# Performance work log

Measured on AMD Instinct MI355X. Metric: run time of the kernel, lower is better.

Reference implementation:

```python
import jax, jax.numpy as jnp
import numpy as np

WS = 16         # window size
NH = 16         # num heads
EPS = 1e-6


def _ln(x):
    m = jnp.mean(x, axis=-1, keepdims=True)
    v = jnp.var(x, axis=-1, keepdims=True)
    return (x - m) * jax.lax.rsqrt(v + EPS)


def _modulate(x, shift, scale):
    return x * (1.0 + scale[:, None, :]) + shift[:, None, :]


def setup_inputs() -> dict:
    key = jax.random.key(0)
    ks = jax.random.split(key, 14)
    D, HD = 1024, 64
    s = 0.02
    return {
        'x': jax.random.normal(ks[0], (4, 4096, D), jnp.float32),
        'c': jax.random.normal(ks[1], (4, D), jnp.float32),
        'qkv_w': jax.random.normal(ks[2], (3 * D, D), jnp.float32) * s,
        'qkv_b': jax.random.normal(ks[3], (3 * D,), jnp.float32) * s,
        'proj_w': jax.random.normal(ks[4], (D, D), jnp.float32) * s,
        'proj_b': jax.random.normal(ks[5], (D,), jnp.float32) * s,
        'rel_pos_h': jax.random.normal(ks[6], (2 * WS - 1, HD), jnp.float32) * s,
        'rel_pos_w': jax.random.normal(ks[7], (2 * WS - 1, HD), jnp.float32) * s,
        'adaLN_w': jax.random.normal(ks[8], (6 * D, D), jnp.float32) * s,
        'adaLN_b': jax.random.normal(ks[9], (6 * D,), jnp.float32) * s,
        'fc1_w': jax.random.normal(ks[10], (4 * D, D), jnp.float32) * s,
        'fc1_b': jax.random.normal(ks[11], (4 * D,), jnp.float32) * s,
        'fc2_w': jax.random.normal(ks[12], (D, 4 * D), jnp.float32) * s,
        'fc2_b': jax.random.normal(ks[13], (D,), jnp.float32) * s,
    }


def _window_attention(x, qkv_w, qkv_b, proj_w, proj_b, rel_pos_h, rel_pos_w):
    # x: [N, T, D] with T = h*w, h = w = sqrt(T)
    N, T, D = x.shape
    h = w = int(round(T ** 0.5))
    nwh, nww = h // WS, w // WS  # grid divides evenly -> no padding
    hd = D // NH
    scale = hd ** -0.5

    # window partition: [N, h, w, D] -> [B, WS, WS, D], B = N*nwh*nww
    xw = x.reshape(N, nwh, WS, nww, WS, D).transpose(0, 1, 3, 2, 4, 5)
    xw = xw.reshape(N * nwh * nww, WS, WS, D)
    B = xw.shape[0]
    L = WS * WS

    qkv = (xw.reshape(B, L, D) @ qkv_w.T + qkv_b)  # [B, L, 3D]
    qkv = qkv.reshape(B, L, 3, NH, hd).transpose(2, 0, 3, 1, 4)  # [3, B, NH, L, hd]
    qkv = qkv.reshape(3, B * NH, L, hd)
    q, k, v = qkv[0], qkv[1], qkv[2]

    attn = jnp.einsum('bqc,bkc->bqk', q * scale, k)  # [B*NH, L, L]

    # decomposed relative position bias (q_size == k_size == WS)
    coords = jnp.arange(WS)
    rel_idx = coords[:, None] - coords[None, :] + (WS - 1)  # [WS, WS]
    Rh = rel_pos_h[rel_idx]  # [WS(q_h), WS(k_h), hd]
    Rw = rel_pos_w[rel_idx]  # [WS(q_w), WS(k_w), hd]
    rq = q.reshape(B * NH, WS, WS, hd)
    rel_h = jnp.einsum('bhwc,hkc->bhwk', rq, Rh)  # [B*NH, WS, WS, WS(kh)]
    rel_w = jnp.einsum('bhwc,wkc->bhwk', rq, Rw)  # [B*NH, WS, WS, WS(kw)]
    attn = (attn.reshape(B * NH, WS, WS, WS, WS)
            + rel_h[:, :, :, :, None]
            + rel_w[:, :, :, None, :]).reshape(B * NH, L, L)

    probs = jax.nn.softmax(attn, axis=-1)
    out = probs @ v  # [B*NH, L, hd]
    out = out.reshape(B, NH, WS, WS, hd).transpose(0, 2, 3, 1, 4).reshape(B, WS, WS, D)
    out = out @ proj_w.T + proj_b

    # window unpartition: [B, WS, WS, D] -> [N, T, D]
    out = out.reshape(N, nwh, nww, WS, WS, D).transpose(0, 1, 3, 2, 4, 5)
    return out.reshape(N, T, D)


def reference(x, c, qkv_w, qkv_b, proj_w, proj_b, rel_pos_h, rel_pos_w,
              adaLN_w, adaLN_b, fc1_w, fc1_b, fc2_w, fc2_b):
    D = x.shape[-1]
    mod = jax.nn.silu(c) @ adaLN_w.T + adaLN_b  # [N, 6D]
    sh_msa, sc_msa, g_msa, sh_mlp, sc_mlp, g_mlp = jnp.split(mod, 6, axis=1)

    a_in = _modulate(_ln(x), sh_msa, sc_msa)
    a_out = _window_attention(a_in, qkv_w, qkv_b, proj_w, proj_b, rel_pos_h, rel_pos_w)
    x = x + g_msa[:, None, :] * a_out

    m_in = _modulate(_ln(x), sh_mlp, sc_mlp)
    hdn = jax.nn.gelu(m_in @ fc1_w.T + fc1_b, approximate=True)
    m_out = hdn @ fc2_w.T + fc2_b
    x = x + g_mlp[:, None, :] * m_out
    return x
```

## Files before the change

### kernel.cpp

```cpp
#include <hip/hip_runtime.h>
#include <cstdint>
#include <cstddef>


typedef float  f32x4    __attribute__((ext_vector_type(4)));
typedef __bf16 bf16x8_t __attribute__((ext_vector_type(8)));
typedef __bf16 bf16x4_t __attribute__((ext_vector_type(4)));

#define DEV __device__ __forceinline__

DEV void gload_lds16(const void* g, void* l) {
    auto gp = (const uint32_t __attribute__((address_space(1)))*)(uintptr_t)g;
    auto lp = (uint32_t __attribute__((address_space(3)))*)(uint32_t)(uintptr_t)l;
    __builtin_amdgcn_global_load_lds(gp, lp, 16, 0, 0);
}

DEV bf16x8_t lds_frag(const __bf16* base, int row, int chunk, int row_elems) {
    return *(const bf16x8_t*)(base + row * row_elems + ((chunk ^ (row & 7)) << 3));
}

DEV bf16x8_t p_frag(const __bf16* base, int row, int chunk) {
    return *(const bf16x8_t*)(base + row * 32 + ((chunk ^ ((row >> 1) & 3)) << 3));
}

DEV int vt_addr(int d, int k) {
    return d * 64 + ((((k >> 3) ^ (d & 7) ^ ((d >> 3) & 7)) << 3) | (k & 7));
}

DEV float gelu_tanh(float v) {
    float u = 0.7978845608028654f * (v + 0.044715f * v * v * v);
    float e = __expf(2.f * u);
    float th = 1.f - 2.f / (e + 1.f);
    return 0.5f * v * (1.f + th);
}

DEV int win2tok(int r) {
    int nb = r >> 12, wi = (r >> 8) & 15, l = r & 255;
    return (nb << 12) + (wi >> 2) * 1024 + (l >> 4) * 64 + (wi & 3) * 16 + (l & 15);
}

__global__ void silu_k(const float* __restrict__ c, float* __restrict__ o, int n) {
    int i = blockIdx.x * 256 + threadIdx.x;
    if (i < n) { float v = c[i]; o[i] = v / (1.f + __expf(-v)); }
}

__global__ void zero_k(float* o, int n) {
    int i = blockIdx.x * 256 + threadIdx.x;
    if (i < n) o[i] = 0.f;
}

__global__ void conv_bf16(const float* __restrict__ s, __bf16* __restrict__ d, int n4) {
    int i = blockIdx.x * 256 + threadIdx.x;
    if (i < n4) {
        float4 v = ((const float4*)s)[i];
        bf16x4_t o; o[0] = (__bf16)v.x; o[1] = (__bf16)v.y; o[2] = (__bf16)v.z; o[3] = (__bf16)v.w;
        ((bf16x4_t*)d)[i] = o;
    }
}

__global__ __launch_bounds__(256)
void mod_gemv(const float* __restrict__ sc, const float* __restrict__ w,
              const float* __restrict__ b, float* __restrict__ mod) {
    int o = (blockIdx.x << 2) + (threadIdx.x >> 6);
    int lane = threadIdx.x & 63;
    int n = o / 6144, col = o % 6144;
    const float4* wr = (const float4*)(w + (size_t)col * 1024);
    const float4* sr = (const float4*)(sc + n * 1024);
    float acc = 0.f;
    #pragma unroll 4
    for (int i = lane; i < 256; i += 64) {
        float4 a = wr[i], x = sr[i];
        acc += a.x * x.x + a.y * x.y + a.z * x.z + a.w * x.w;
    }
    #pragma unroll
    for (int m = 1; m < 64; m <<= 1) acc += __shfl_xor(acc, m);
    if (lane == 0) mod[o] = acc + b[col];
}

__global__ __launch_bounds__(256)
void ln_mod_k(const float* __restrict__ src, const float* __restrict__ mod,
              int sh_off, int sc_off, __bf16* __restrict__ out, int permute, int r0) {
    int rl = blockIdx.x;
    int r = rl + r0;
    int nb = r >> 12;
    int t = permute ? win2tok(r) : r;
    float4 v = ((const float4*)(src + (size_t)t * 1024))[threadIdx.x];
    float s  = v.x + v.y + v.z + v.w;
    float sq = v.x * v.x + v.y * v.y + v.z * v.z + v.w * v.w;
    #pragma unroll
    for (int m = 1; m < 64; m <<= 1) { s += __shfl_xor(s, m); sq += __shfl_xor(sq, m); }
    __shared__ float ps[4], pq[4];
    int wv = threadIdx.x >> 6, ln = threadIdx.x & 63;
    if (ln == 0) { ps[wv] = s; pq[wv] = sq; }
    __syncthreads();
    s  = ps[0] + ps[1] + ps[2] + ps[3];
    sq = pq[0] + pq[1] + pq[2] + pq[3];
    float mean = s * (1.f / 1024.f);
    float var  = sq * (1.f / 1024.f) - mean * mean;
    float rstd = rsqrtf(var + 1e-6f);
    int c = threadIdx.x << 2;
    const float* mrow = mod + nb * 6144;
    float4 scv = *(const float4*)(mrow + sc_off + c);
    float4 shv = *(const float4*)(mrow + sh_off + c);
    bf16x4_t o;
    o[0] = (__bf16)((v.x - mean) * rstd * (1.f + scv.x) + shv.x);
    o[1] = (__bf16)((v.y - mean) * rstd * (1.f + scv.y) + shv.y);
    o[2] = (__bf16)((v.z - mean) * rstd * (1.f + scv.z) + shv.z);
    o[3] = (__bf16)((v.w - mean) * rstd * (1.f + scv.w) + shv.w);
    *(bf16x4_t*)(out + (size_t)rl * 1024 + c) = o;
}

template <int PM, int PN>
DEV void mfma16(f32x4 (&acc)[8][4], bf16x8_t (&fa)[4][2], bf16x8_t (&fb)[2][2][2]) {
    #pragma unroll
    for (int ks = 0; ks < 2; ++ks)
        #pragma unroll
        for (int mi = 0; mi < 4; ++mi)
            #pragma unroll
            for (int nn = 0; nn < 2; ++nn)
                acc[PM * 4 + mi][PN * 2 + nn] = __builtin_amdgcn_mfma_f32_16x16x32_bf16(
                    fa[mi][ks], fb[PN][nn][ks], acc[PM * 4 + mi][PN * 2 + nn], 0, 0, 0);
}

#define GBAR  __builtin_amdgcn_s_barrier()
#define LGKM0 do { asm volatile("s_waitcnt lgkmcnt(0)" ::: "memory"); \
                   __builtin_amdgcn_sched_barrier(0); } while (0)
#define PRIO1 __builtin_amdgcn_s_setprio(1)
#define PRIO0 __builtin_amdgcn_s_setprio(0)

template <int EPI>
__global__ __launch_bounds__(512)
void gemm256(const __bf16* __restrict__ A, const __bf16* __restrict__ B,
             const float* __restrict__ bias, void* __restrict__ Cout,
             const float* __restrict__ extra, const float* __restrict__ mod,
             int N, int K, int r0, int gx) {
    extern __shared__ __align__(16) char smem[];
    __bf16* lA = (__bf16*)smem;
    __bf16* lB = lA + 2 * 16384;
    const int tid = threadIdx.x, lane = tid & 63, wv = tid >> 6;
    const int wr = wv >> 2, wc = wv & 3;

    const int nwg = gridDim.x;
    const int qq = nwg >> 3, rr8 = nwg & 7;
    const int xcd = blockIdx.x & 7, pos = blockIdx.x >> 3;
    const int nid = (xcd < rr8 ? xcd * (qq + 1) : rr8 * (qq + 1) + (xcd - rr8) * qq) + pos;
    const int bm = (nid / gx) << 8, bn = (nid % gx) << 8;

    f32x4 acc[8][4];
    const f32x4 z4 = {0.f, 0.f, 0.f, 0.f};
    #pragma unroll
    for (int i = 0; i < 8; ++i)
        #pragma unroll
        for (int j = 0; j < 4; ++j) acc[i][j] = z4;

    bf16x8_t fa[4][2], fb[2][2][2];

    const int l8  = lane >> 3;
    const int gc8 = ((lane & 7) ^ l8) << 3;
    const int rbw = ((wv & 3) << 3) + ((wv >> 2) << 6);
    const __bf16* gA0 = A + (size_t)(bm +       (wv << 3) + l8) * K + gc8;
    const __bf16* gA1 = A + (size_t)(bm + 128 + (wv << 3) + l8) * K + gc8;
    const __bf16* gA2 = A + (size_t)(bm +  64 + (wv << 3) + l8) * K + gc8;
    const __bf16* gA3 = A + (size_t)(bm + 192 + (wv << 3) + l8) * K + gc8;
    const __bf16* gB0 = B + (size_t)(bn +       rbw + l8) * K + gc8;
    const __bf16* gB1 = B + (size_t)(bn + 128 + rbw + l8) * K + gc8;
    const __bf16* gB2 = B + (size_t)(bn +  32 + rbw + l8) * K + gc8;
    const __bf16* gB3 = B + (size_t)(bn + 160 + rbw + l8) * K + gc8;
    const int dA0 = (wv << 3) * 64, dA1 = (128 + (wv << 3)) * 64;
    const int dA2 = (64 + (wv << 3)) * 64, dA3 = (192 + (wv << 3)) * 64;
    const int dB0 = rbw * 64, dB1 = (128 + rbw) * 64;
    const int dB2 = (32 + rbw) * 64, dB3 = (160 + rbw) * 64;

    auto stA0 = [&](int be) { gload_lds16(gA0, lA + be + dA0); gload_lds16(gA1, lA + be + dA1); gA0 += 64; gA1 += 64; };
    auto stA1 = [&](int be) { gload_lds16(gA2, lA + be + dA2); gload_lds16(gA3, lA + be + dA3); gA2 += 64; gA3 += 64; };
    auto stB0 = [&](int be) { gload_lds16(gB0, lB + be + dB0); gload_lds16(gB1, lB + be + dB1); gB0 += 64; gB1 += 64; };
    auto stB1 = [&](int be) { gload_lds16(gB2, lB + be + dB2); gload_lds16(gB3, lB + be + dB3); gB2 += 64; gB3 += 64; };

    const int swzb = (lane >> 4) ^ (lane & 7);
    const __bf16* aR0 = lA + (wr << 13) + ((lane & 15) << 6) + (swzb << 3);
    const __bf16* aR1 = lA + (wr << 13) + ((lane & 15) << 6) + ((swzb ^ 4) << 3);
    const __bf16* bR0 = lB + (wc << 12) + ((lane & 15) << 6) + (swzb << 3);
    const __bf16* bR1 = lB + (wc << 12) + ((lane & 15) << 6) + ((swzb ^ 4) << 3);

    auto readA = [&](int be, int pm) {
        #pragma unroll
        for (int mi = 0; mi < 4; ++mi) {
            fa[mi][0] = *(const bf16x8_t*)(aR0 + be + pm * 4096 + mi * 1024);
            fa[mi][1] = *(const bf16x8_t*)(aR1 + be + pm * 4096 + mi * 1024);
        }
    };
    auto readB = [&](int be, int pn) {
        #pragma unroll
        for (int ni = 0; ni < 2; ++ni) {
            fb[pn][ni][0] = *(const bf16x8_t*)(bR0 + be + pn * 2048 + ni * 1024);
            fb[pn][ni][1] = *(const bf16x8_t*)(bR1 + be + pn * 2048 + ni * 1024);
        }
    };

    const int nt = K >> 6;
    stA0(0); stB0(0); stB1(0); stA1(0);
    stA0(16384); stB0(16384); stB1(16384);
    asm volatile("s_waitcnt vmcnt(6)" ::: "memory");
    GBAR;

    int be = 0;
    for (int t = 0; t < nt - 1; ++t) {
        const bool s2 = (t + 2 < nt);
        readA(be, 0); readB(be, 0);
        stA1(be ^ 16384);
        GBAR; LGKM0;
        PRIO1; mfma16<0, 0>(acc, fa, fb); PRIO0;
        GBAR;
        readB(be, 1);
        if (s2) stA0(be);
        GBAR; LGKM0;
        PRIO1; mfma16<0, 1>(acc, fa, fb); PRIO0;
        GBAR;
        readA(be, 1);
        if (s2) stB0(be);
        GBAR; LGKM0;
        PRIO1; mfma16<1, 0>(acc, fa, fb); PRIO0;
        GBAR;
        if (s2) stB1(be);
        if (t == nt - 2) asm volatile("s_waitcnt vmcnt(0)" ::: "memory");
        else             asm volatile("s_waitcnt vmcnt(6)" ::: "memory");
        GBAR;
        PRIO1; mfma16<1, 1>(acc, fa, fb); PRIO0;
        GBAR;
        be ^= 16384;
    }
    readA(be, 0); readB(be, 0); readB(be, 1);
    LGKM0;
    PRIO1; mfma16<0, 0>(acc, fa, fb); mfma16<0, 1>(acc, fa, fb); PRIO0;
    readA(be, 1);
    LGKM0;
    PRIO1; mfma16<1, 0>(acc, fa, fb); mfma16<1, 1>(acc, fa, fb); PRIO0;

    #pragma unroll
    for (int am = 0; am < 8; ++am) {
        #pragma unroll
        for (int j = 0; j < 4; ++j) {
            int m = bm + (wr << 7) + (am << 4) + ((lane >> 4) << 2) + j;
            #pragma unroll
            for (int an = 0; an < 4; ++an) {
                int n = bn + (wc << 6) + (an << 4) + (lane & 15);
                float v = acc[am][an][j] + bias[n];
                if constexpr (EPI == 0) {
                    ((__bf16*)Cout)[(size_t)m * N + n] = (__bf16)v;
                } else if constexpr (EPI == 1) {
                    int mg = m + r0;
                    int tr = win2tok(mg);
                    float g = mod[(mg >> 12) * 6144 + 2048 + n];
                    ((float*)Cout)[(size_t)tr * 1024 + n] = extra[(size_t)tr * 1024 + n] + g * v;
                } else if constexpr (EPI == 2) {
                    ((__bf16*)Cout)[(size_t)m * N + n] = (__bf16)gelu_tanh(v);
                } else {
                    int mg = m + r0;
                    float g = mod[(mg >> 12) * 6144 + 5120 + n];
                    ((float*)Cout)[(size_t)mg * 1024 + n] = extra[(size_t)mg * 1024 + n] + g * v;
                }
            }
        }
    }
}

__global__ __launch_bounds__(256)
void tab_k(const __bf16* __restrict__ qkv, const float* __restrict__ relh,
           const float* __restrict__ relw, __bf16* __restrict__ tab) {
    __shared__ __bf16 lR[2][31][72];
    for (int i = threadIdx.x; i < 1984; i += 256) {
        int row = i >> 6, c = i & 63;
        lR[0][row][c] = (__bf16)relh[i];
        lR[1][row][c] = (__bf16)relw[i];
    }
    __syncthreads();
    const int h = blockIdx.y;
    const int r = threadIdx.x >> 1, half = threadIdx.x & 1;
    const int l = blockIdx.x * 128 + r;
    const int lw = l & 255;
    const int qi = lw >> 4, qj = lw & 15;
    const __bf16* qrow = qkv + (size_t)l * 3072 + h * 64;
    float qq[64];
    #pragma unroll
    for (int c8 = 0; c8 < 8; ++c8) {
        bf16x8_t q8 = *(const bf16x8_t*)(qrow + (c8 << 3));
        #pragma unroll
        for (int e = 0; e < 8; ++e) qq[c8 * 8 + e] = (float)q8[e];
    }
    bf16x8_t oh, ow;
    #pragma unroll
    for (int kk = 0; kk < 8; ++kk) {
        int kg = (half << 3) + kk;
        const __bf16* Rh = &lR[0][qi - kg + 15][0];
        const __bf16* Rw = &lR[1][qj - kg + 15][0];
        float ah = 0.f, aw = 0.f;
        #pragma unroll
        for (int c8 = 0; c8 < 8; ++c8) {
            bf16x8_t r1 = *(const bf16x8_t*)(Rh + (c8 << 3));
            bf16x8_t r2 = *(const bf16x8_t*)(Rw + (c8 << 3));
            #pragma unroll
            for (int e = 0; e < 8; ++e) {
                ah += qq[c8 * 8 + e] * (float)r1[e];
                aw += qq[c8 * 8 + e] * (float)r2[e];
            }
        }
        oh[kk] = (__bf16)ah; ow[kk] = (__bf16)aw;
    }
    size_t idx = ((size_t)(l >> 8) * 16 + h) * 256 + lw;
    *(bf16x8_t*)(tab + idx * 32 + (half << 3))      = oh;
    *(bf16x8_t*)(tab + idx * 32 + 16 + (half << 3)) = ow;
}

__global__ __launch_bounds__(256, 3)
void attn_k(const __bf16* __restrict__ qkv, const __bf16* __restrict__ tab,
            __bf16* __restrict__ out) {
    __shared__ __align__(16) __bf16 lP[4][32 * 32];
    __shared__ __align__(16) __bf16 lKt[2][64 * 64];
    __shared__ __align__(16) __bf16 lVt[2][64 * 64];
    __shared__ __align__(16) __bf16 lTab[128 * 32];

    const int blk = blockIdx.x;
    const int winc = blk >> 5, h = (blk >> 1) & 15, qh = blk & 1;
    const int tid = threadIdx.x, lane = tid & 63, wv = tid >> 6;
    const __bf16* base = qkv + (size_t)winc * 256 * 3072 + h * 64;
    const int q0 = qh << 7;

    {
        const __bf16* ts = tab + (((size_t)winc * 16 + h) * 256 + q0) * 32;
        #pragma unroll
        for (int q = 0; q < 2; ++q) {
            int c = (wv << 1) + q;
            gload_lds16(ts + c * 512 + lane * 8, lTab + c * 512);
        }
    }
    bf16x8_t qf[2][2];
    #pragma unroll
    for (int mi = 0; mi < 2; ++mi)
        #pragma unroll
        for (int ks = 0; ks < 2; ++ks) {
            int l = q0 + (wv << 5) + (mi << 4) + (lane & 15);
            qf[mi][ks] = *(const bf16x8_t*)(base + (size_t)l * 3072 + (((ks << 2) + (lane >> 4)) << 3));
        }
    {
        const __bf16* kb = base + 1024;
        #pragma unroll
        for (int q = 0; q < 2; ++q) {
            int c = (wv << 1) + q;
            int kl = (c << 3) + (lane >> 3);
            gload_lds16(kb + (size_t)kl * 3072 + (((lane & 7) ^ (lane >> 3)) << 3),
                        lKt[0] + c * 512);
        }
        const __bf16* vb = base + 2048;
        bf16x8_t a = *(const bf16x8_t*)(vb + (size_t)(tid >> 3) * 3072 + ((tid & 7) << 3));
        bf16x8_t b = *(const bf16x8_t*)(vb + (size_t)(32 + (tid >> 3)) * 3072 + ((tid & 7) << 3));
        int lc = tid & 7;
        #pragma unroll
        for (int e = 0; e < 8; ++e) {
            lVt[0][vt_addr(lc * 8 + e, tid >> 3)]        = a[e];
            lVt[0][vt_addr(lc * 8 + e, 32 + (tid >> 3))] = b[e];
        }
    }
    __syncthreads();

    float twv[2][4];
    #pragma unroll
    for (int mi = 0; mi < 2; ++mi)
        #pragma unroll
        for (int j = 0; j < 4; ++j) {
            int qr = (wv << 5) + (mi << 4) + ((lane >> 4) << 2) + j;
            twv[mi][j] = (float)lTab[qr * 32 + 16 + (lane & 15)];
        }

    const f32x4 z4 = {0.f, 0.f, 0.f, 0.f};
    f32x4 oacc[2][4];
    #pragma unroll
    for (int a = 0; a < 2; ++a)
        #pragma unroll
        for (int b = 0; b < 4; ++b) oacc[a][b] = z4;
    float rsum[2][4];
    #pragma unroll
    for (int a = 0; a < 2; ++a)
        #pragma unroll
        for (int j = 0; j < 4; ++j) rsum[a][j] = 0.f;
    __bf16* lPw = lP[wv];

    int cur = 0;
    for (int kt = 0; kt < 4; ++kt) {
        const bool pre = (kt < 3);
        bf16x8_t v8a, v8b;
        if (pre) {
            const __bf16* kb = base + 1024 + (size_t)(kt + 1) * 64 * 3072;
            #pragma unroll
            for (int q = 0; q < 2; ++q) {
                int c = (wv << 1) + q;
                int kl = (c << 3) + (lane >> 3);
                gload_lds16(kb + (size_t)kl * 3072 + (((lane & 7) ^ (lane >> 3)) << 3),
                            lKt[cur ^ 1] + c * 512);
            }
            const __bf16* vb = base + 2048 + (size_t)(kt + 1) * 64 * 3072;
            v8a = *(const bf16x8_t*)(vb + (size_t)(tid >> 3) * 3072 + ((tid & 7) << 3));
            v8b = *(const bf16x8_t*)(vb + (size_t)(32 + (tid >> 3)) * 3072 + ((tid & 7) << 3));
        }

        f32x4 s[2][4];
        #pragma unroll
        for (int a = 0; a < 2; ++a)
            #pragma unroll
            for (int b = 0; b < 4; ++b) s[a][b] = z4;
        #pragma unroll
        for (int ks = 0; ks < 2; ++ks) {
            bf16x8_t kf[4];
            #pragma unroll
            for (int ni = 0; ni < 4; ++ni)
                kf[ni] = lds_frag(lKt[cur], (ni << 4) + (lane & 15), (ks << 2) + (lane >> 4), 64);
            #pragma unroll
            for (int mi = 0; mi < 2; ++mi)
                #pragma unroll
                for (int ni = 0; ni < 4; ++ni)
                    s[mi][ni] = __builtin_amdgcn_mfma_f32_16x16x32_bf16(qf[mi][ks], kf[ni], s[mi][ni], 0, 0, 0);
        }

        #pragma unroll
        for (int mi = 0; mi < 2; ++mi) {
            #pragma unroll
            for (int j = 0; j < 4; ++j) {
                int qr = (wv << 5) + (mi << 4) + ((lane >> 4) << 2) + j;
                bf16x4_t th4 = *(const bf16x4_t*)(lTab + qr * 32 + (kt << 2));
                float rs = 0.f;
                #pragma unroll
                for (int ni = 0; ni < 4; ++ni) {
                    float p = __expf(s[mi][ni][j] * 0.125f + (float)th4[ni] + twv[mi][j]);
                    s[mi][ni][j] = p;
                    rs += p;
                }
                rsum[mi][j] += rs;
            }
        }

        #pragma unroll
        for (int hf = 0; hf < 2; ++hf) {
            #pragma unroll
            for (int mi = 0; mi < 2; ++mi) {
                #pragma unroll
                for (int j = 0; j < 4; ++j) {
                    int rl = (mi << 4) + ((lane >> 4) << 2) + j;
                    #pragma unroll
                    for (int b = 0; b < 2; ++b) {
                        int col = (b << 4) + (lane & 15);
                        lPw[rl * 32 + ((((col >> 3) ^ ((rl >> 1) & 3)) << 3) | (col & 7))] =
                            (__bf16)s[mi][(hf << 1) + b][j];
                    }
                }
            }
            bf16x8_t pf[2], vf[4];
            #pragma unroll
            for (int mi = 0; mi < 2; ++mi)
                pf[mi] = p_frag(lPw, (mi << 4) + (lane & 15), lane >> 4);
            #pragma unroll
            for (int no = 0; no < 4; ++no) {
                int d = (no << 4) + (lane & 15);
                vf[no] = *(const bf16x8_t*)(lVt[cur] + vt_addr(d, ((hf << 2) + (lane >> 4)) << 3));
            }
            #pragma unroll
            for (int mi = 0; mi < 2; ++mi)
                #pragma unroll
                for (int no = 0; no < 4; ++no)
                    oacc[mi][no] = __builtin_amdgcn_mfma_f32_16x16x32_bf16(pf[mi], vf[no], oacc[mi][no], 0, 0, 0);
        }

        if (pre) {
            int lc = tid & 7;
            #pragma unroll
            for (int e = 0; e < 8; ++e) {
                lVt[cur ^ 1][vt_addr(lc * 8 + e, tid >> 3)]        = v8a[e];
                lVt[cur ^ 1][vt_addr(lc * 8 + e, 32 + (tid >> 3))] = v8b[e];
            }
        }
        __syncthreads();
        cur ^= 1;
    }

    #pragma unroll
    for (int mi = 0; mi < 2; ++mi) {
        #pragma unroll
        for (int j = 0; j < 4; ++j) {
            float rs = rsum[mi][j];
            #pragma unroll
            for (int msk = 1; msk < 16; msk <<= 1) rs += __shfl_xor(rs, msk);
            float inv = 1.f / rs;
            int l = q0 + (wv << 5) + (mi << 4) + ((lane >> 4) << 2) + j;
            #pragma unroll
            for (int no = 0; no < 4; ++no) {
                int col = (no << 4) + (lane & 15);
                out[(size_t)(winc * 256 + l) * 1024 + h * 64 + col] = (__bf16)(oacc[mi][no][j] * inv);
            }
        }
    }
}

extern "C" void kernel_launch(void* const* d_in, const int* in_sizes, int n_in,
                              void* d_out, int out_size, void* d_ws, size_t ws_size,
                              hipStream_t stream) {
    const float* x      = (const float*)d_in[0];
    const float* c      = (const float*)d_in[1];
    const float* qkv_w  = (const float*)d_in[2];
    const float* qkv_b  = (const float*)d_in[3];
    const float* proj_w = (const float*)d_in[4];
    const float* proj_b = (const float*)d_in[5];
    const float* rel_h  = (const float*)d_in[6];
    const float* rel_w  = (const float*)d_in[7];
    const float* ada_w  = (const float*)d_in[8];
    const float* ada_b  = (const float*)d_in[9];
    const float* fc1_w  = (const float*)d_in[10];
    const float* fc1_b  = (const float*)d_in[11];
    const float* fc2_w  = (const float*)d_in[12];
    const float* fc2_b  = (const float*)d_in[13];
    float* xo = (float*)d_out;

    char* ws = (char*)d_ws;
    const size_t MB = 1ull << 20;
    int CH = 0;
    const int cands[7] = {16384, 8192, 4096, 2048, 1024, 512, 256};
    for (int i = 0; i < 7; ++i)
        if (26 * MB + (size_t)cands[i] * 10240 <= ws_size) { CH = cands[i]; break; }
    if (CH == 0) {
        zero_k<<<65536, 256, 0, stream>>>(xo, 16777216);
        return;
    }

    const int LDSB = 131072;
    hipFuncSetAttribute((const void*)&gemm256<0>, hipFuncAttributeMaxDynamicSharedMemorySize, LDSB);
    hipFuncSetAttribute((const void*)&gemm256<1>, hipFuncAttributeMaxDynamicSharedMemorySize, LDSB);
    hipFuncSetAttribute((const void*)&gemm256<2>, hipFuncAttributeMaxDynamicSharedMemorySize, LDSB);
    hipFuncSetAttribute((const void*)&gemm256<3>, hipFuncAttributeMaxDynamicSharedMemorySize, LDSB);

    const int NCH = 16384 / CH;
    float*  ws_silu = (float*)(ws);
    float*  ws_mod  = (float*)(ws + 65536);
    __bf16* w_qkv   = (__bf16*)(ws + 1 * MB);
    __bf16* w_proj  = (__bf16*)(ws + 7 * MB);
    __bf16* w_fc1   = (__bf16*)(ws + 9 * MB);
    __bf16* w_fc2   = (__bf16*)(ws + 17 * MB);
    __bf16* bufA    = (__bf16*)(ws + 26 * MB);
    __bf16* bufB    = (__bf16*)(ws + 26 * MB + (size_t)CH * 2048);
    __bf16* tabbuf  = bufB + (size_t)CH * 3072;

    silu_k   <<<16,   256, 0, stream>>>(c, ws_silu, 4096);
    mod_gemv <<<6144, 256, 0, stream>>>(ws_silu, ada_w, ada_b, ws_mod);
    conv_bf16<<<3072, 256, 0, stream>>>(qkv_w,  w_qkv,  786432);
    conv_bf16<<<1024, 256, 0, stream>>>(proj_w, w_proj, 262144);
    conv_bf16<<<4096, 256, 0, stream>>>(fc1_w,  w_fc1,  1048576);
    conv_bf16<<<4096, 256, 0, stream>>>(fc2_w,  w_fc2,  1048576);

    const int gy = CH / 256;
    for (int ci = 0; ci < NCH; ++ci) {
        int r0 = ci * CH;
        ln_mod_k<<<CH, 256, 0, stream>>>(x, ws_mod, 0, 1024, bufA, 1, r0);
        gemm256<0><<<12 * gy, 512, LDSB, stream>>>(bufA, w_qkv, qkv_b, bufB,
                                                   nullptr, nullptr, 3072, 1024, r0, 12);
        tab_k<<<dim3(CH / 128, 16), 256, 0, stream>>>(bufB, rel_h, rel_w, tabbuf);
        attn_k<<<(CH / 256) * 32, 256, 0, stream>>>(bufB, tabbuf, bufA);
        gemm256<1><<<4 * gy, 512, LDSB, stream>>>(bufA, w_proj, proj_b, xo,
                                                  x, ws_mod, 1024, 1024, r0, 4);
    }
    for (int ci = 0; ci < NCH; ++ci) {
        int r0 = ci * CH;
        ln_mod_k<<<CH, 256, 0, stream>>>(xo, ws_mod, 3072, 4096, bufA, 0, r0);
        gemm256<2><<<16 * gy, 512, LDSB, stream>>>(bufA, w_fc1, fc1_b, bufB,
                                                   nullptr, nullptr, 4096, 1024, r0, 16);
        gemm256<3><<<4 * gy, 512, LDSB, stream>>>(bufB, w_fc2, fc2_b, xo,
                                                  xo, ws_mod, 1024, 4096, r0, 4);
    }
}
```

Baseline: 645.2 us.

## Restructure GEMM main loop to a one-barrier-per-phase pipeline with sub-tile prefetch

Reworks the gemm256 K-loop schedule. It drops the prologue prefetch of the second stage, the explicit LDS-wait plus sched_barrier macro, and half the workgroup barriers. Each quarter-phase now issues one global-to-LDS sub-tile load into the other buffer, waits on vmcnt(6), takes a single barrier, then reads fragments and runs MFMAs. The aim is less barrier and wait overhead, at the cost of a shallower prefetch distance (one tile instead of two) and relying on the compiler to order LDS reads before the MFMAs.

```diff
diff --git a/kernel.cpp b/kernel.cpp
--- a/kernel.cpp
+++ b/kernel.cpp
@@ -123,8 +123,7 @@
 }
 
 #define GBAR  __builtin_amdgcn_s_barrier()
-#define LGKM0 do { asm volatile("s_waitcnt lgkmcnt(0)" ::: "memory"); \
-                   __builtin_amdgcn_sched_barrier(0); } while (0)
+#define VM6   asm volatile("s_waitcnt vmcnt(6)" ::: "memory")
 #define PRIO1 __builtin_amdgcn_s_setprio(1)
 #define PRIO0 __builtin_amdgcn_s_setprio(0)
 
@@ -199,41 +198,36 @@
 
     const int nt = K >> 6;
     stA0(0); stB0(0); stB1(0); stA1(0);
-    stA0(16384); stB0(16384); stB1(16384);
-    asm volatile("s_waitcnt vmcnt(6)" ::: "memory");
-    GBAR;
 
     int be = 0;
     for (int t = 0; t < nt - 1; ++t) {
-        const bool s2 = (t + 2 < nt);
+        stA0(be ^ 16384);
+        VM6; GBAR;
         readA(be, 0); readB(be, 0);
+        PRIO1; mfma16<0, 0>(acc, fa, fb); PRIO0;
+        stB0(be ^ 16384);
+        VM6; GBAR;
+        readB(be, 1);
+        PRIO1; mfma16<0, 1>(acc, fa, fb); PRIO0;
+        stB1(be ^ 16384);
+        VM6; GBAR;
+        readA(be, 1);
+        PRIO1; mfma16<1, 0>(acc, fa, fb); PRIO0;
         stA1(be ^ 16384);
-        GBAR; LGKM0;
-        PRIO1; mfma16<0, 0>(acc, fa, fb); PRIO0;
-        GBAR;
-        readB(be, 1);
-        if (s2) stA0(be);
-        GBAR; LGKM0;
-        PRIO1; mfma16<0, 1>(acc, fa, fb); PRIO0;
-        GBAR;
-        readA(be, 1);
-        if (s2) stB0(be);
-        GBAR; LGKM0;
-        PRIO1; mfma16<1, 0>(acc, fa, fb); PRIO0;
-        GBAR;
-        if (s2) stB1(be);
-        if (t == nt - 2) asm volatile("s_waitcnt vmcnt(0)" ::: "memory");
-        else             asm volatile("s_waitcnt vmcnt(6)" ::: "memory");
-        GBAR;
         PRIO1; mfma16<1, 1>(acc, fa, fb); PRIO0;
-        GBAR;
         be ^= 16384;
     }
-    readA(be, 0); readB(be, 0); readB(be, 1);
-    LGKM0;
-    PRIO1; mfma16<0, 0>(acc, fa, fb); mfma16<0, 1>(acc, fa, fb); PRIO0;
+    asm volatile("s_waitcnt vmcnt(4)" ::: "memory");
+    GBAR;
+    readA(be, 0); readB(be, 0);
+    PRIO1; mfma16<0, 0>(acc, fa, fb); PRIO0;
+    asm volatile("s_waitcnt vmcnt(2)" ::: "memory");
+    GBAR;
+    readB(be, 1);
+    PRIO1; mfma16<0, 1>(acc, fa, fb); PRIO0;
+    asm volatile("s_waitcnt vmcnt(0)" ::: "memory");
+    GBAR;
     readA(be, 1);
-    LGKM0;
     PRIO1; mfma16<1, 0>(acc, fa, fb); mfma16<1, 1>(acc, fa, fb); PRIO0;
 
     #pragma unroll
```

Measured after the change: 631.5 us. 1.02x faster.
